# Performance work log

Hardware: AMD Instinct MI355X
Metric: run time of the kernel (lower is better)

Reference implementation:

```python
import jax, jax.numpy as jnp
import numpy as np

HID = 2048
NH = 16
NKV = 16
HD = HID // NH          # 128
ROPE_BASE = 100000.0
ROPE_SCALE = 4.0
B, L = 2, 2048
NEG = -1e9


def rope(x, offset=0):
    # x: [B, NH, L, HD]; half-split (rotate-half) RoPE with linear scaling
    Lx = x.shape[2]
    D = HD // 2
    pos = (jnp.arange(offset, offset + Lx, dtype=jnp.float32) / ROPE_SCALE)  # [L]
    freq = jnp.exp(-jnp.arange(D, dtype=jnp.float32) * (np.log(ROPE_BASE) / D))  # [D]
    m_theta = pos[:, None] * freq[None, :]          # [L, D]
    cos, sin = jnp.cos(m_theta), jnp.sin(m_theta)
    x1, x2 = x[..., :D], x[..., D:]
    rx1 = x1 * cos - x2 * sin
    rx2 = x1 * sin + x2 * cos
    return jnp.concatenate([rx1, rx2], axis=-1)


def setup_inputs() -> dict:
    key = jax.random.key(0)
    ks = jax.random.split(key, 5)
    x = jax.random.normal(ks[0], (B, L, HID), dtype=jnp.float32)
    # additive causal mask [1,1,L,L]
    mask = jnp.triu(jnp.full((L, L), NEG, dtype=jnp.float32), k=1)[None, None]
    Wq = jax.random.normal(ks[1], (HID, NH * HD), dtype=jnp.float32) * 0.02
    Wk = jax.random.normal(ks[2], (HID, NKV * HD), dtype=jnp.float32) * 0.02
    Wv = jax.random.normal(ks[3], (HID, NKV * HD), dtype=jnp.float32) * 0.02
    Wo = jax.random.normal(ks[4], (NH * HD, HID), dtype=jnp.float32) * 0.02
    return {"x": x, "mask": mask, "Wq": Wq, "Wk": Wk, "Wv": Wv, "Wo": Wo}


def reference(x, mask, Wq, Wk, Wv, Wo):
    b, l, _ = x.shape
    scale = HD ** -0.5
    q = (x @ Wq).reshape(b, l, NH, HD).transpose(0, 2, 1, 3)    # [B,NH,L,HD]
    k = (x @ Wk).reshape(b, l, NKV, HD).transpose(0, 2, 1, 3)
    v = (x @ Wv).reshape(b, l, NKV, HD).transpose(0, 2, 1, 3)
    rep = NH // NKV
    if rep > 1:
        k = jnp.repeat(k, rep, axis=1)
        v = jnp.repeat(v, rep, axis=1)
    q = rope(q)
    k = rope(k)
    scores = scale * jnp.einsum('bhqd,bhkd->bhqk', q, k)        # [B,NH,L,L]
    scores = scores + mask
    attn = jax.nn.softmax(scores, axis=-1)
    out = jnp.einsum('bhqk,bhkd->bhqd', attn, v)                # [B,NH,L,HD]
    out = out.transpose(0, 2, 1, 3).reshape(b, l, NH * HD)
    return out @ Wo
```

## Files before the change

kernel.cpp:

```cpp
#include <hip/hip_runtime.h>
#include <math.h>

#define BB   2
#define LL   2048
#define HIDD 2048
#define NHH  16
#define HDD  128
#define QKVN 6144
#define THR2 11.5416f

typedef unsigned short u16;
typedef float  f32x4 __attribute__((ext_vector_type(4)));
typedef __bf16 bf16x8 __attribute__((ext_vector_type(8)));

static __device__ __forceinline__ float exp2_fast(float x){
  return __builtin_amdgcn_exp2f(x);
}
static __device__ __forceinline__ u16 f2bf(float x){
  unsigned u = __float_as_uint(x);
  return (u16)((u + 0x7fffu + ((u >> 16) & 1u)) >> 16);
}
static __device__ __forceinline__ float bf2f(u16 b){
  return __uint_as_float(((unsigned)b) << 16);
}
static __device__ __forceinline__ void gl_lds16(const void* g, void* l){
  __builtin_amdgcn_global_load_lds(
      (__attribute__((address_space(1))) void*)(void*)g,
      (__attribute__((address_space(3))) void*)l,
      16, 0, 0);
}


__global__ void cvt_f32_bf16_k(const float* __restrict__ src, u16* __restrict__ dst, int n4){
  int i = blockIdx.x * blockDim.x + threadIdx.x;
  if (i >= n4) return;
  float4 v = ((const float4*)src)[i];
  ushort4 o;
  o.x = f2bf(v.x); o.y = f2bf(v.y); o.z = f2bf(v.z); o.w = f2bf(v.w);
  ((ushort4*)dst)[i] = o;
}

__global__ __launch_bounds__(256) void transpose_cvt4_k(
    const float* __restrict__ Wq, const float* __restrict__ Wk,
    const float* __restrict__ Wv, const float* __restrict__ Wo,
    u16* __restrict__ Wt, u16* __restrict__ Wot)
{
  __shared__ u16 t[64][66];
  const int z = blockIdx.z;
  const float* src = (z == 0) ? Wq : (z == 1) ? Wk : (z == 2) ? Wv : Wo;
  u16* dst = (z == 3) ? Wot : (Wt + (size_t)z * 2048 * 2048);
  const int c0 = blockIdx.x * 64, r0 = blockIdx.y * 64;
  const int tid = threadIdx.x;

  #pragma unroll
  for (int i = 0; i < 4; i++){
    int r  = i * 16 + (tid >> 4);
    int c4 = (tid & 15) * 4;
    float4 v = *(const float4*)&src[(size_t)(r0 + r) * 2048 + c0 + c4];
    t[c4 + 0][r] = f2bf(v.x);
    t[c4 + 1][r] = f2bf(v.y);
    t[c4 + 2][r] = f2bf(v.z);
    t[c4 + 3][r] = f2bf(v.w);
  }
  __syncthreads();
  #pragma unroll
  for (int i = 0; i < 2; i++){
    int c  = i * 32 + (tid >> 3);
    int rs = (tid & 7) * 8;
    const unsigned* p = (const unsigned*)&t[c][rs];
    unsigned w0 = p[0], w1 = p[1], w2 = p[2], w3 = p[3];
    u16* d = &dst[(size_t)(c0 + c) * 2048 + r0 + rs];
    ((unsigned*)d)[0] = w0; ((unsigned*)d)[1] = w1;
    ((unsigned*)d)[2] = w2; ((unsigned*)d)[3] = w3;
  }
}

__global__ void rope_k(u16* __restrict__ qkv){
  int idx = blockIdx.x * blockDim.x + threadIdx.x;
  int d   = idx & 63;
  int h   = (idx >> 6) & 15;
  int row = idx >> 10;
  int l   = row & (LL - 1);
  float fr = __expf(-(float)d * 0.17988946f);
  float th = (float)l * 0.25f * fr;
  float s, c;
  sincosf(th, &s, &c);
  size_t base = (size_t)row * QKVN + h * HDD + d;
  #pragma unroll
  for (int part = 0; part < 2; part++){
    float f = (part == 0) ? 0.12753375f : 1.0f;
    float x1 = bf2f(qkv[base]), x2 = bf2f(qkv[base + 64]);
    qkv[base]      = f2bf((x1 * c - x2 * s) * f);
    qkv[base + 64] = f2bf((x1 * s + x2 * c) * f);
    base += HIDD;
  }
}

__global__ void build_vt_k(const u16* __restrict__ qkv, u16* __restrict__ vt){
  __shared__ u16 t[32][33];
  int bh = blockIdx.z;
  int b = bh >> 4, h = bh & 15;
  const u16* src = qkv + (size_t)b * LL * QKVN + 2 * HIDD + h * HDD;
  u16* dst = vt + (size_t)bh * HDD * LL;
  int d0 = blockIdx.x * 32, l0 = blockIdx.y * 32;
  int tx = threadIdx.x, ty = threadIdx.y;
  #pragma unroll
  for (int i = 0; i < 32; i += 8) t[ty + i][tx] = src[(size_t)(l0 + ty + i) * QKVN + d0 + tx];
  __syncthreads();
  #pragma unroll
  for (int i = 0; i < 32; i += 8) dst[(size_t)(d0 + ty + i) * LL + l0 + tx] = t[tx][ty + i];
}


template<int OUT_BF16>
__global__ __launch_bounds__(256) void gemm_bt_k(
    const u16* __restrict__ A, const u16* __restrict__ Bt,
    void* __restrict__ Cout, int M, int N, int K)
{
  __shared__ __align__(16) u16 As[128 * 64];
  __shared__ __align__(16) u16 Bs[128 * 64];
  const int tid = threadIdx.x, lane = tid & 63, wv = tid >> 6;
  const int wr = wv >> 1, wc = wv & 1;
  const int m0 = blockIdx.y * 128, n0 = blockIdx.x * 128;
  const int rq = lane >> 4, cl = lane & 15;

  const f32x4 Z = {0.f, 0.f, 0.f, 0.f};
  f32x4 acc[4][4];
  #pragma unroll
  for (int m = 0; m < 4; m++)
    #pragma unroll
    for (int n = 0; n < 4; n++) acc[m][n] = Z;

  for (int kt = 0; kt < K; kt += 64){
    #pragma unroll
    for (int i = 0; i < 4; i++){
      int fb = (i * 4 + wv) * 64;
      int p  = (fb + lane) * 16;
      int r  = p >> 7;
      int cbs = (p & 127) ^ ((r & 7) << 4);
      gl_lds16(A  + (size_t)(m0 + r) * K + kt + (cbs >> 1), &As[fb * 8]);
      gl_lds16(Bt + (size_t)(n0 + r) * K + kt + (cbs >> 1), &Bs[fb * 8]);
    }
    __syncthreads();
    #pragma unroll
    for (int ks = 0; ks < 2; ks++){
      const int kb = ks * 64 + rq * 16;
      bf16x8 a[4], b[4];
      #pragma unroll
      for (int m = 0; m < 4; m++){
        int r = wr * 64 + m * 16 + cl;
        a[m] = *(const bf16x8*)((const char*)As + r * 128 + (kb ^ ((r & 7) << 4)));
      }
      #pragma unroll
      for (int n = 0; n < 4; n++){
        int r = wc * 64 + n * 16 + cl;
        b[n] = *(const bf16x8*)((const char*)Bs + r * 128 + (kb ^ ((r & 7) << 4)));
      }
      #pragma unroll
      for (int m = 0; m < 4; m++)
        #pragma unroll
        for (int n = 0; n < 4; n++)
          acc[m][n] = __builtin_amdgcn_mfma_f32_16x16x32_bf16(a[m], b[n], acc[m][n], 0, 0, 0);
    }
    __syncthreads();
  }

  #pragma unroll
  for (int m = 0; m < 4; m++){
    int gr0 = m0 + wr * 64 + m * 16 + rq * 4;
    #pragma unroll
    for (int n = 0; n < 4; n++){
      int gc = n0 + wc * 64 + n * 16 + cl;
      #pragma unroll
      for (int rr = 0; rr < 4; rr++){
        if (OUT_BF16) ((u16*)Cout)[(size_t)(gr0 + rr) * N + gc] = f2bf(acc[m][n][rr]);
        else          ((float*)Cout)[(size_t)(gr0 + rr) * N + gc] = acc[m][n][rr];
      }
    }
  }
}


#define G2_STAGE(kt, bsel) do {                                                           \
  _Pragma("unroll")                                                                       \
  for (int i_ = 0; i_ < 2; i_++){                            \
    int c_ = ((i_ * 8 + wv) * 64) + lane;                                                 \
    int p_ = c_ * 16;                                                                     \
    int r_ = p_ >> 7; int cb_ = (p_ & 127) ^ ((r_ & 7) << 4);                             \
    gl_lds16(A + (size_t)(m0 + r_) * K + (kt) + (cb_ >> 1),                               \
             &AB[bsel][((i_ * 8 + wv) * 64) * 8]);                                        \
  }                                                                                       \
  _Pragma("unroll")                                                                       \
  for (int i_ = 0; i_ < 4; i_++){                            \
    int c_ = ((i_ * 8 + wv) * 64) + lane;                                                 \
    int p_ = c_ * 16;                                                                     \
    int r_ = p_ >> 7; int cb_ = (p_ & 127) ^ ((r_ & 7) << 4);                             \
    gl_lds16(Bt + (size_t)(n0 + r_) * K + (kt) + (cb_ >> 1),                              \
             &AB[bsel][8192 + ((i_ * 8 + wv) * 64) * 8]);                                 \
  }                                                                                       \
} while(0)

template<int OUT_BF16>
__global__ __launch_bounds__(512, 1) void gemm_bt2_k(
    const u16* __restrict__ A, const u16* __restrict__ Bt,
    void* __restrict__ Cout, int M, int N, int K)
{
  __shared__ __align__(16) u16 AB[2][24576];
  const int tid = threadIdx.x, lane = tid & 63, wv = tid >> 6;
  const int wr = wv >> 2, wc = wv & 3;
  const int m0 = blockIdx.y * 128, n0 = blockIdx.x * 256;
  const int rq = lane >> 4, cl = lane & 15;
  const int NT = K >> 6;

  const f32x4 Z = {0.f, 0.f, 0.f, 0.f};
  f32x4 acc[4][4];
  #pragma unroll
  for (int m = 0; m < 4; m++)
    #pragma unroll
    for (int n = 0; n < 4; n++) acc[m][n] = Z;

  G2_STAGE(0, 0);
  G2_STAGE(64, 1);
  asm volatile("s_waitcnt vmcnt(6)");
  __builtin_amdgcn_sched_barrier(0);
  __builtin_amdgcn_s_barrier();

  int cur = 0;
  for (int t = 0; t < NT; t++){
    const char* As_ = (const char*)&AB[cur][0];
    const char* Bs_ = (const char*)&AB[cur][8192];

    #pragma unroll
    for (int ks = 0; ks < 2; ks++){
      const int kb = ks * 64 + rq * 16;
      bf16x8 a[4], b[4];
      #pragma unroll
      for (int m = 0; m < 4; m++){
        int r = wr * 64 + m * 16 + cl;
        a[m] = *(const bf16x8*)(As_ + r * 128 + (kb ^ ((r & 7) << 4)));
      }
      #pragma unroll
      for (int n = 0; n < 4; n++){
        int r = wc * 64 + n * 16 + cl;
        b[n] = *(const bf16x8*)(Bs_ + r * 128 + (kb ^ ((r & 7) << 4)));
      }
      __builtin_amdgcn_s_setprio(1);
      #pragma unroll
      for (int m = 0; m < 4; m++)
        #pragma unroll
        for (int n = 0; n < 4; n++)
          acc[m][n] = __builtin_amdgcn_mfma_f32_16x16x32_bf16(a[m], b[n], acc[m][n], 0, 0, 0);
      __builtin_amdgcn_s_setprio(0);
    }

    __builtin_amdgcn_sched_barrier(0);
    __builtin_amdgcn_s_barrier();

    if (t + 2 < NT){
      G2_STAGE((t + 2) * 64, cur);
      asm volatile("s_waitcnt vmcnt(6)");
    } else {
      asm volatile("s_waitcnt vmcnt(0)");
    }
    __builtin_amdgcn_sched_barrier(0);
    __builtin_amdgcn_s_barrier();
    cur ^= 1;
  }

  #pragma unroll
  for (int m = 0; m < 4; m++){
    int gr0 = m0 + wr * 64 + m * 16 + rq * 4;
    #pragma unroll
    for (int n = 0; n < 4; n++){
      int gc = n0 + wc * 64 + n * 16 + cl;
      #pragma unroll
      for (int rr = 0; rr < 4; rr++){
        if (OUT_BF16) ((u16*)Cout)[(size_t)(gr0 + rr) * N + gc] = f2bf(acc[m][n][rr]);
        else          ((float*)Cout)[(size_t)(gr0 + rr) * N + gc] = acc[m][n][rr];
      }
    }
  }
}


#define STAGE_K(jj, bsel) do {                                                            \
  _Pragma("unroll")                                                                       \
  for (int i_ = 0; i_ < 4; i_++){                                                         \
    int fb_ = (i_ * 4 + wv) * 64;                                                         \
    int p_  = (fb_ + lane) * 16;                                                          \
    int r_ = p_ >> 8; int cb_ = (p_ & 255) ^ ((r_ & 7) << 4);                             \
    gl_lds16(qkv + (size_t)(b * LL + (jj) * 64 + r_) * QKVN + HIDD + h * HDD + (cb_ >> 1),\
             &Kb[bsel][fb_ * 8]);                                                         \
  }                                                                                       \
} while(0)

#define STAGE_V(jj) do {                                                                  \
  _Pragma("unroll")                                                                       \
  for (int i_ = 0; i_ < 4; i_++){                                                         \
    int fb_ = (i_ * 4 + wv) * 64;                                                         \
    int p_  = (fb_ + lane) * 16;                                                          \
    int r_ = p_ >> 7; int cb_ = (p_ & 127) ^ ((r_ & 7) << 4);                             \
    gl_lds16(vt + (size_t)(bh * HDD + r_) * LL + (jj) * 64 + (cb_ >> 1), &Vs[fb_ * 8]);   \
  }                                                                                       \
} while(0)

__global__ __launch_bounds__(256, 2) void attn_k(
    const u16* __restrict__ qkv, const u16* __restrict__ vt,
    u16* __restrict__ aout)
{
  __shared__ __align__(16) u16 Kb[2][64 * 128];
  __shared__ __align__(16) u16 Vs[128 * 64];
  __shared__ __align__(16) u16 Ps[4][1024];
  const int tid = threadIdx.x, lane = tid & 63, wv = tid >> 6;
  const int bh = blockIdx.x;
  const int pr = blockIdx.y;
  const int b = bh >> 4, h = bh & 15;
  const int rq = lane >> 4, cl = lane & 15;

  bf16x8 ones;
  #pragma unroll
  for (int i = 0; i < 8; i++) ones[i] = (__bf16)1.0f;
  const f32x4 Z = {0.f, 0.f, 0.f, 0.f};

  int cur = 0;
  STAGE_K(0, 0);
  asm volatile("s_waitcnt vmcnt(0)" ::: "memory");
  __builtin_amdgcn_sched_barrier(0);
  __builtin_amdgcn_s_barrier();

  #pragma unroll
  for (int ph = 0; ph < 2; ph++){
    const int qt = ph ? pr : (31 - pr);
    const int nj = qt + 1;

    bf16x8 qf[4];
    {
      const u16* qb = qkv + (size_t)(b * LL + qt * 64 + wv * 16 + cl) * QKVN + h * HDD + rq * 8;
      #pragma unroll
      for (int ks = 0; ks < 4; ks++) qf[ks] = *(const bf16x8*)(qb + ks * 32);
    }

    f32x4 acco[8], accl;
    float mst[4];
    #pragma unroll
    for (int n = 0; n < 8; n++) acco[n] = Z;
    accl = Z;
    #pragma unroll
    for (int rr = 0; rr < 4; rr++) mst[rr] = -INFINITY;

    for (int j = 0; j < nj; j++){
      const bool sn = (j + 1 < nj) || (ph == 0);
      STAGE_V(j);
      if (j + 1 < nj)      STAGE_K(j + 1, cur ^ 1);
      else if (ph == 0)    STAGE_K(0,     cur ^ 1);
      __builtin_amdgcn_sched_barrier(0);
      if (sn) asm volatile("s_waitcnt vmcnt(8)" ::: "memory");
      else    asm volatile("s_waitcnt vmcnt(4)" ::: "memory");
      __builtin_amdgcn_sched_barrier(0);
      __builtin_amdgcn_s_barrier();
      __builtin_amdgcn_sched_barrier(0);

      f32x4 sv[4];
      {
        const char* KsC = (const char*)&Kb[cur][0];
        #pragma unroll
        for (int ct = 0; ct < 4; ct++) sv[ct] = Z;
        #pragma unroll
        for (int ks = 0; ks < 4; ks++){
          const int kb = ks * 64 + rq * 16;
          #pragma unroll
          for (int ct = 0; ct < 4; ct++){
            int r = ct * 16 + cl;
            bf16x8 bfr = *(const bf16x8*)(KsC + r * 256 + (kb ^ ((r & 7) << 4)));
            sv[ct] = __builtin_amdgcn_mfma_f32_16x16x32_bf16(qf[ks], bfr, sv[ct], 0, 0, 0);
          }
        }
      }

      {
        char* pbase = (char*)&Ps[wv][0];
        const bool msk = (j == qt);

        float p4[4][4], lmx[4];
        #pragma unroll
        for (int rr = 0; rr < 4; rr++) lmx[rr] = -1e30f;
        const int qg = qt * 64 + wv * 16 + rq * 4;
        #pragma unroll
        for (int ct = 0; ct < 4; ct++){
          int col = j * 64 + ct * 16 + cl;
          #pragma unroll
          for (int rr = 0; rr < 4; rr++){
            float v = sv[ct][rr];
            if (msk && col > qg + rr) v = -1e30f;
            p4[ct][rr] = v;
            lmx[rr] = fmaxf(lmx[rr], v);
          }
        }
        float need = -1e30f;
        #pragma unroll
        for (int rr = 0; rr < 4; rr++) need = fmaxf(need, lmx[rr] - mst[rr]);
        if (__any(need > THR2)){
          float mx[4];
          #pragma unroll
          for (int rr = 0; rr < 4; rr++) mx[rr] = lmx[rr];
          #pragma unroll
          for (int off = 1; off < 16; off <<= 1)
            #pragma unroll
            for (int rr = 0; rr < 4; rr++)
              mx[rr] = fmaxf(mx[rr], __shfl_xor(mx[rr], off, 64));
          #pragma unroll
          for (int rr = 0; rr < 4; rr++){
            float mn  = fmaxf(mst[rr], mx[rr]);
            float fsc = exp2_fast(mst[rr] - mn);
            mst[rr] = mn;
            accl[rr] *= fsc;
            #pragma unroll
            for (int n = 0; n < 8; n++) acco[n][rr] *= fsc;
          }
        }
        #pragma unroll
        for (int ct = 0; ct < 4; ct++)
          #pragma unroll
          for (int rr = 0; rr < 4; rr++){
            float e = exp2_fast(p4[ct][rr] - mst[rr]);
            int wr = rq * 4 + rr;
            *(u16*)(pbase + wr * 128 + (((ct * 16 + cl) * 2) ^ ((wr & 7) << 4))) = f2bf(e);
          }
      }

      __builtin_amdgcn_sched_barrier(0);
      if (sn) asm volatile("s_waitcnt vmcnt(4)" ::: "memory");
      else    asm volatile("s_waitcnt vmcnt(0)" ::: "memory");
      __builtin_amdgcn_sched_barrier(0);
      __builtin_amdgcn_s_barrier();
      __builtin_amdgcn_sched_barrier(0);

      {
        const char* VsC = (const char*)Vs;
        char* pbase = (char*)&Ps[wv][0];
        #pragma unroll
        for (int ks = 0; ks < 2; ks++){
          const int kvb = ks * 64 + rq * 16;
          bf16x8 pa = *(const bf16x8*)(pbase + cl * 128 + (kvb ^ ((cl & 7) << 4)));
          accl = __builtin_amdgcn_mfma_f32_16x16x32_bf16(pa, ones, accl, 0, 0, 0);
          #pragma unroll
          for (int n = 0; n < 8; n++){
            int r = n * 16 + cl;
            bf16x8 bfr = *(const bf16x8*)(VsC + r * 128 + (kvb ^ ((r & 7) << 4)));
            acco[n] = __builtin_amdgcn_mfma_f32_16x16x32_bf16(pa, bfr, acco[n], 0, 0, 0);
          }
        }
      }

      __builtin_amdgcn_sched_barrier(0);
      __builtin_amdgcn_s_barrier();
      __builtin_amdgcn_sched_barrier(0);
      cur ^= 1;
    }

    #pragma unroll
    for (int rr = 0; rr < 4; rr++){
      float inv = 1.0f / accl[rr];
      size_t grow = (size_t)(b * LL + qt * 64 + wv * 16 + rq * 4 + rr);
      #pragma unroll
      for (int n = 0; n < 8; n++)
        aout[grow * HIDD + h * HDD + n * 16 + cl] = f2bf(acco[n][rr] * inv);
    }
  }
}


extern "C" void kernel_launch(void* const* d_in, const int* in_sizes, int n_in,
                              void* d_out, int out_size, void* d_ws, size_t ws_size,
                              hipStream_t stream)
{
  const float* x  = (const float*)d_in[0];
  const float* Wq = (const float*)d_in[2];
  const float* Wk = (const float*)d_in[3];
  const float* Wv = (const float*)d_in[4];
  const float* Wo = (const float*)d_in[5];
  float* out = (float*)d_out;

  if (ws_size < 134217728ull) return;

  char* ws = (char*)d_ws;
  u16* xb   = (u16*)(ws);
  u16* Wt   = (u16*)(ws + 16777216ull);
  u16* Wot  = (u16*)(ws + 41943040ull);
  u16* qkv  = (u16*)(ws + 50331648ull);
  u16* vt   = (u16*)(ws + 100663296ull);
  u16* aout = (u16*)(ws + 117440512ull);

  cvt_f32_bf16_k<<<2097152 / 256, 256, 0, stream>>>(x, xb, 2097152);
  transpose_cvt4_k<<<dim3(32, 32, 4), 256, 0, stream>>>(Wq, Wk, Wv, Wo, Wt, Wot);

  gemm_bt_k<1><<<dim3(6144 / 128, 4096 / 128), 256, 0, stream>>>(xb, Wt, qkv, 4096, 6144, 2048);
  rope_k<<<4194304 / 256, 256, 0, stream>>>(qkv);
  build_vt_k<<<dim3(4, 64, 32), dim3(32, 8), 0, stream>>>(qkv, vt);

  attn_k<<<dim3(32, 16), 256, 0, stream>>>(qkv, vt, aout);

  gemm_bt2_k<0><<<dim3(2048 / 256, 4096 / 128), 512, 0, stream>>>(aout, Wot, out, 4096, 2048, 2048);
}
```

Baseline: 265.0 us.

## Fuse RoPE and V transpose into QKV GEMM epilogue via LDS staging

The QKV projection GEMM now stages its output tile in shared memory and applies RoPE (with a precomputed cos/sin table) to Q and K, or writes V already transposed into the vt layout. This removes the separate rope and build_vt kernels and their extra global round trips over the QKV buffer. In exchange the GEMM epilogue gets extra LDS traffic and a barrier, and a small table kernel is added. Q/K are now stored in a narrower 4096-column buffer.

```diff
diff --git a/kernel.cpp b/kernel.cpp
--- a/kernel.cpp
+++ b/kernel.cpp
@@ -6,7 +6,7 @@
 #define HIDD 2048
 #define NHH  16
 #define HDD  128
-#define QKVN 6144
+#define QKN  4096
 #define THR2 11.5416f
 
 typedef unsigned short u16;
@@ -38,6 +38,16 @@
   ushort4 o;
   o.x = f2bf(v.x); o.y = f2bf(v.y); o.z = f2bf(v.z); o.w = f2bf(v.w);
   ((ushort4*)dst)[i] = o;
+}
+
+__global__ void rope_table_k(float2* __restrict__ tab){
+  int idx = blockIdx.x * blockDim.x + threadIdx.x;
+  int l = idx >> 6, d = idx & 63;
+  float fr = __expf(-(float)d * 0.17988946f);
+  float th = (float)l * 0.25f * fr;
+  float s, c;
+  sincosf(th, &s, &c);
+  tab[idx] = make_float2(c, s);
 }
 
 __global__ __launch_bounds__(256) void transpose_cvt4_k(
@@ -75,50 +85,15 @@
   }
 }
 
-__global__ void rope_k(u16* __restrict__ qkv){
-  int idx = blockIdx.x * blockDim.x + threadIdx.x;
-  int d   = idx & 63;
-  int h   = (idx >> 6) & 15;
-  int row = idx >> 10;
-  int l   = row & (LL - 1);
-  float fr = __expf(-(float)d * 0.17988946f);
-  float th = (float)l * 0.25f * fr;
-  float s, c;
-  sincosf(th, &s, &c);
-  size_t base = (size_t)row * QKVN + h * HDD + d;
-  #pragma unroll
-  for (int part = 0; part < 2; part++){
-    float f = (part == 0) ? 0.12753375f : 1.0f;
-    float x1 = bf2f(qkv[base]), x2 = bf2f(qkv[base + 64]);
-    qkv[base]      = f2bf((x1 * c - x2 * s) * f);
-    qkv[base + 64] = f2bf((x1 * s + x2 * c) * f);
-    base += HIDD;
-  }
-}
-
-__global__ void build_vt_k(const u16* __restrict__ qkv, u16* __restrict__ vt){
-  __shared__ u16 t[32][33];
-  int bh = blockIdx.z;
-  int b = bh >> 4, h = bh & 15;
-  const u16* src = qkv + (size_t)b * LL * QKVN + 2 * HIDD + h * HDD;
-  u16* dst = vt + (size_t)bh * HDD * LL;
-  int d0 = blockIdx.x * 32, l0 = blockIdx.y * 32;
-  int tx = threadIdx.x, ty = threadIdx.y;
-  #pragma unroll
-  for (int i = 0; i < 32; i += 8) t[ty + i][tx] = src[(size_t)(l0 + ty + i) * QKVN + d0 + tx];
-  __syncthreads();
-  #pragma unroll
-  for (int i = 0; i < 32; i += 8) dst[(size_t)(d0 + ty + i) * LL + l0 + tx] = t[tx][ty + i];
-}
-
-
-template<int OUT_BF16>
-__global__ __launch_bounds__(256) void gemm_bt_k(
+
+__global__ __launch_bounds__(256) void gemm_qkv_k(
     const u16* __restrict__ A, const u16* __restrict__ Bt,
-    void* __restrict__ Cout, int M, int N, int K)
+    u16* __restrict__ qk, u16* __restrict__ vt,
+    const float2* __restrict__ rtab, int M, int N, int K)
 {
-  __shared__ __align__(16) u16 As[128 * 64];
-  __shared__ __align__(16) u16 Bs[128 * 64];
+  __shared__ __align__(16) u16 SH[16640];
+  u16* As = SH;
+  u16* Bs = SH + 8192;
   const int tid = threadIdx.x, lane = tid & 63, wv = tid >> 6;
   const int wr = wv >> 1, wc = wv & 1;
   const int m0 = blockIdx.y * 128, n0 = blockIdx.x * 128;
@@ -165,17 +140,55 @@
     __syncthreads();
   }
 
+  const int hd  = n0 >> 7;
+  const int sec = hd >> 4;
+  const int hh  = hd & 15;
+
   #pragma unroll
   for (int m = 0; m < 4; m++){
-    int gr0 = m0 + wr * 64 + m * 16 + rq * 4;
+    int gr0 = wr * 64 + m * 16 + rq * 4;
     #pragma unroll
     for (int n = 0; n < 4; n++){
-      int gc = n0 + wc * 64 + n * 16 + cl;
-      #pragma unroll
-      for (int rr = 0; rr < 4; rr++){
-        if (OUT_BF16) ((u16*)Cout)[(size_t)(gr0 + rr) * N + gc] = f2bf(acc[m][n][rr]);
-        else          ((float*)Cout)[(size_t)(gr0 + rr) * N + gc] = acc[m][n][rr];
-      }
+      int gc = wc * 64 + n * 16 + cl;
+      #pragma unroll
+      for (int rr = 0; rr < 4; rr++)
+        SH[(gr0 + rr) * 130 + gc] = f2bf(acc[m][n][rr]);
+    }
+  }
+  __syncthreads();
+
+  if (sec < 2){
+    const float fsc = (sec == 0) ? 0.12753375f : 1.0f;
+    const int r = tid >> 1, dbase = (tid & 1) * 32;
+    const int l = (m0 + r) & (LL - 1);
+    const float2* tab = rtab + l * 64 + dbase;
+    u16* orow = qk + (size_t)(m0 + r) * QKN + hd * 128;
+    #pragma unroll
+    for (int g = 0; g < 4; g++){
+      bf16x8 o1, o2;
+      #pragma unroll
+      for (int i = 0; i < 8; i++){
+        int d = g * 8 + i;
+        float2 cs = tab[d];
+        float x1 = bf2f(SH[r * 130 + dbase + d]);
+        float x2 = bf2f(SH[r * 130 + dbase + d + 64]);
+        o1[i] = (__bf16)((x1 * cs.x - x2 * cs.y) * fsc);
+        o2[i] = (__bf16)((x1 * cs.y + x2 * cs.x) * fsc);
+      }
+      *(bf16x8*)(orow + dbase + g * 8)      = o1;
+      *(bf16x8*)(orow + dbase + 64 + g * 8) = o2;
+    }
+  } else {
+    const int d = tid >> 1, l0 = (tid & 1) * 64;
+    const int bh = ((m0 >> 11) << 4) + hh;
+    u16* vrow = vt + ((size_t)bh * HDD + d) * LL + (m0 & (LL - 1)) + l0;
+    #pragma unroll
+    for (int g = 0; g < 8; g++){
+      bf16x8 o;
+      #pragma unroll
+      for (int i = 0; i < 8; i++)
+        o[i] = *(__bf16*)&SH[(l0 + g * 8 + i) * 130 + d];
+      *(bf16x8*)(vrow + g * 8) = o;
     }
   }
 }
@@ -289,7 +302,7 @@
     int fb_ = (i_ * 4 + wv) * 64;                                                         \
     int p_  = (fb_ + lane) * 16;                                                          \
     int r_ = p_ >> 8; int cb_ = (p_ & 255) ^ ((r_ & 7) << 4);                             \
-    gl_lds16(qkv + (size_t)(b * LL + (jj) * 64 + r_) * QKVN + HIDD + h * HDD + (cb_ >> 1),\
+    gl_lds16(qk + (size_t)(b * LL + (jj) * 64 + r_) * QKN + 2048 + h * HDD + (cb_ >> 1),  \
              &Kb[bsel][fb_ * 8]);                                                         \
   }                                                                                       \
 } while(0)
@@ -305,7 +318,7 @@
 } while(0)
 
 __global__ __launch_bounds__(256, 2) void attn_k(
-    const u16* __restrict__ qkv, const u16* __restrict__ vt,
+    const u16* __restrict__ qk, const u16* __restrict__ vt,
     u16* __restrict__ aout)
 {
   __shared__ __align__(16) u16 Kb[2][64 * 128];
@@ -335,7 +348,7 @@
 
     bf16x8 qf[4];
     {
-      const u16* qb = qkv + (size_t)(b * LL + qt * 64 + wv * 16 + cl) * QKVN + h * HDD + rq * 8;
+      const u16* qb = qk + (size_t)(b * LL + qt * 64 + wv * 16 + cl) * QKN + h * HDD + rq * 8;
       #pragma unroll
       for (int ks = 0; ks < 4; ks++) qf[ks] = *(const bf16x8*)(qb + ks * 32);
     }
@@ -481,24 +494,24 @@
   const float* Wo = (const float*)d_in[5];
   float* out = (float*)d_out;
 
-  if (ws_size < 134217728ull) return;
+  if (ws_size < 120586240ull) return;
 
   char* ws = (char*)d_ws;
-  u16* xb   = (u16*)(ws);
-  u16* Wt   = (u16*)(ws + 16777216ull);
-  u16* Wot  = (u16*)(ws + 41943040ull);
-  u16* qkv  = (u16*)(ws + 50331648ull);
-  u16* vt   = (u16*)(ws + 100663296ull);
-  u16* aout = (u16*)(ws + 117440512ull);
+  u16*    xb   = (u16*)(ws);
+  u16*    Wt   = (u16*)(ws + 16777216ull);
+  u16*    Wot  = (u16*)(ws + 41943040ull);
+  u16*    qk   = (u16*)(ws + 50331648ull);
+  u16*    vt   = (u16*)(ws + 83886080ull);
+  u16*    aout = (u16*)(ws + 100663296ull);
+  float2* rtab = (float2*)(ws + 117440512ull);
 
   cvt_f32_bf16_k<<<2097152 / 256, 256, 0, stream>>>(x, xb, 2097152);
+  rope_table_k<<<131072 / 256, 256, 0, stream>>>(rtab);
   transpose_cvt4_k<<<dim3(32, 32, 4), 256, 0, stream>>>(Wq, Wk, Wv, Wo, Wt, Wot);
 
-  gemm_bt_k<1><<<dim3(6144 / 128, 4096 / 128), 256, 0, stream>>>(xb, Wt, qkv, 4096, 6144, 2048);
-  rope_k<<<4194304 / 256, 256, 0, stream>>>(qkv);
-  build_vt_k<<<dim3(4, 64, 32), dim3(32, 8), 0, stream>>>(qkv, vt);
-
-  attn_k<<<dim3(32, 16), 256, 0, stream>>>(qkv, vt, aout);
+  gemm_qkv_k<<<dim3(6144 / 128, 4096 / 128), 256, 0, stream>>>(xb, Wt, qk, vt, rtab, 4096, 6144, 2048);
+
+  attn_k<<<dim3(32, 16), 256, 0, stream>>>(qk, vt, aout);
 
   gemm_bt2_k<0><<<dim3(2048 / 256, 4096 / 128), 512, 0, stream>>>(aout, Wot, out, 4096, 2048, 2048);
 }
```

New measurement: 261.3 us. Within noise of the previous version (-1.4%).
